# Kernel tuning notes

Measured on AMD Instinct MI355X. Metric: run time of the kernel, lower is better.

Reference implementation:

```python
import jax, jax.numpy as jnp
import numpy as np

B, S, D = 16, 2048, 400
HEADS, HEAD_SIZE = 4, 100
SCALE = 1.0 / np.float32(100.0 ** 0.5)


def setup_inputs() -> dict:
    key = jax.random.key(0)
    ks = jax.random.split(key, 8)
    return {
        "x": jax.random.normal(ks[0], (B, S, D), jnp.float32),
        "attn_kernel": jax.random.normal(ks[1], (3, D, HEAD_SIZE), jnp.float32) * 0.05,
        "attn_dense": jax.random.normal(ks[2], (D, HEADS * HEAD_SIZE), jnp.float32) * 0.05,
        "d1_w": jax.random.normal(ks[3], (400, 400), jnp.float32) * 0.05,
        "d1_b": jnp.zeros((400,), jnp.float32),
        "fc1_w": jax.random.normal(ks[4], (800, 512), jnp.float32) * 0.05,
        "fc1_b": jnp.zeros((512,), jnp.float32),
        "fc2_w": jax.random.normal(ks[5], (512, 256), jnp.float32) * 0.05,
        "fc2_b": jnp.zeros((256,), jnp.float32),
    }


def reference(x, attn_kernel, attn_dense, d1_w, d1_b, fc1_w, fc1_b, fc2_w, fc2_b):
    # Multi-head attention. NOTE: the original loops `heads` times over the SAME
    # shared kernel, so all 4 head outputs are identical; compute once, tile.
    WQ = jnp.einsum('bsd,dh->bsh', x, attn_kernel[0])  # [B,S,100]
    WK = jnp.einsum('bsd,dh->bsh', x, attn_kernel[1])
    WV = jnp.einsum('bsd,dh->bsh', x, attn_kernel[2])
    scores = jnp.einsum('bqh,bkh->bqk', WQ, WK) * SCALE  # [B,S,S]
    probs = jax.nn.softmax(scores, axis=-1)
    V = jnp.einsum('bqk,bkh->bqh', probs, WV)  # [B,S,100]
    out = jnp.tile(V, (1, 1, HEADS))  # concat of identical heads -> [B,S,400]
    out = jnp.einsum('bsd,de->bse', out, attn_dense)  # [B,S,400]
    # Dropout layers are identity at inference.
    h = jax.nn.relu(jnp.einsum('bsd,de->bse', out, d1_w) + d1_b)  # [B,S,400]
    pooled = jnp.concatenate([jnp.max(h, axis=1), jnp.mean(h, axis=1)], axis=-1)  # [B,800]
    h = jax.nn.relu(pooled @ fc1_w + fc1_b)  # [B,512]
    h = jax.nn.relu(h @ fc2_w + fc2_b)  # [B,256]
    return h
```

## Files before the change

### kernel.cpp

```cpp
#include <hip/hip_runtime.h>

typedef __attribute__((ext_vector_type(8))) _Float16 f16x8;
typedef __attribute__((ext_vector_type(4))) float f4v;
typedef __attribute__((ext_vector_type(8))) unsigned short us8;
typedef __attribute__((ext_vector_type(4))) unsigned short us4;
typedef unsigned short u16;

__device__ __forceinline__ u16 h2b(_Float16 h) { return __builtin_bit_cast(u16, h); }
__device__ __forceinline__ float b2f(u16 b) {
    return (float)__builtin_bit_cast(_Float16, b);
}

#define BAR() do { asm volatile("s_waitcnt lgkmcnt(0)" ::: "memory"); \
                   __builtin_amdgcn_s_barrier(); } while (0)

__global__ void k_w2p(const float* __restrict__ ad, const float* __restrict__ d1w,
                      float* __restrict__ w2p) {
    int i = blockIdx.x * 256 + threadIdx.x;
    if (i >= 51200) return;
    int es = blockIdx.y;
    int d = i / 400, j = i % 400;
    float acc = 0.f;
    if (d < 100) {
        const float* a0 = ad + d * 400 + es * 100;
        const float* wr = d1w + (es * 100) * 400 + j;
        #pragma unroll 4
        for (int e = 0; e < 100; ++e) {
            float av = a0[e] + a0[40000 + e] + a0[80000 + e] + a0[120000 + e];
            acc += av * wr[e * 400];
        }
    }
    w2p[es * 51200 + i] = acc;
}

__global__ void k_w2r(const float* __restrict__ w2p, u16* __restrict__ w2f) {
    int i = blockIdx.x * 256 + threadIdx.x;
    if (i >= 51200) return;
    float acc = w2p[i] + w2p[51200 + i] + w2p[102400 + i] + w2p[153600 + i];
    int d = i / 400, j = i % 400;
    int idx = ((j >> 4) * 4 + (d >> 5)) * 512 + (((d >> 3) & 3) * 16 + (j & 15)) * 8 + (d & 7);
    w2f[idx] = h2b((_Float16)acc);
}

__global__ void k_wprep(const float* __restrict__ ak, u16* __restrict__ wsp) {
    int i = blockIdx.x * 256 + threadIdx.x;
    if (i >= 159744) return;
    int k = i & 31, n = (i >> 5) & 127;
    int xx = i >> 12;
    int ks = xx % 13, m = xx / 13;
    int gk = ks * 32 + k;
    float v = (n < 100 && gk < 400) ? ak[m * 40000 + gk * 100 + n] : 0.f;
    _Float16 hb = (_Float16)v;
    _Float16 lb = (_Float16)(v - (float)hb);
    long base = (long)xx * 8192;
    int pos = n * 32 + ((((k >> 3) ^ (n & 3)) << 3) | (k & 7));
    wsp[base + pos] = h2b(hb);
    wsp[base + 4096 + pos] = h2b(lb);
}

__global__ __launch_bounds__(512) void k_gemm_qkv(
    const float* __restrict__ x, const u16* __restrict__ wsp,
    u16* __restrict__ QH, u16* __restrict__ KH, u16* __restrict__ VT) {
    __shared__ __align__(16) u16 smem[49152];

    const int tid = threadIdx.x;
    const int rowblk = blockIdx.x;
    const long row0 = (long)rowblk * 128;
    const int w = tid >> 6, l = tid & 63, g = l >> 4, c15 = l & 15;
    const int sr = tid >> 2, skc = tid & 3;

    f4v aQ[8], aK[8], aV[8];
    #pragma unroll
    for (int nt = 0; nt < 8; ++nt) {
        aQ[nt] = (f4v){0.f, 0.f, 0.f, 0.f};
        aK[nt] = (f4v){0.f, 0.f, 0.f, 0.f};
        aV[nt] = (f4v){0.f, 0.f, 0.f, 0.f};
    }

    const u16* wq  = wsp;
    const u16* wkh = wsp + 106496;
    const u16* wkl = wsp + 110592;
    const u16* wv  = wsp + 212992;

    float4 xr0, xr1;
    us8 wr[4];
    const int xpos = sr * 32 + ((skc * 8) ^ ((sr & 3) << 3));

    {
        const float* xp = x + (row0 + sr) * 400 + skc * 8;
        xr0 = *(const float4*)xp;
        xr1 = *(const float4*)(xp + 4);
        wr[0] = *(const us8*)&wq [(long)tid * 8];
        wr[1] = *(const us8*)&wkh[(long)tid * 8];
        wr[2] = *(const us8*)&wkl[(long)tid * 8];
        wr[3] = *(const us8*)&wv [(long)tid * 8];
        float va[8] = {xr0.x, xr0.y, xr0.z, xr0.w, xr1.x, xr1.y, xr1.z, xr1.w};
        us8 hi8, lo8;
        #pragma unroll
        for (int j = 0; j < 8; ++j) {
            _Float16 h = (_Float16)va[j];
            hi8[j] = h2b(h);
            lo8[j] = h2b((_Float16)(va[j] - (float)h));
        }
        *(us8*)&smem[xpos] = hi8;
        *(us8*)&smem[4096 + xpos] = lo8;
        *(us8*)&smem[8192  + tid * 8] = wr[0];
        *(us8*)&smem[12288 + tid * 8] = wr[1];
        *(us8*)&smem[16384 + tid * 8] = wr[2];
        *(us8*)&smem[20480 + tid * 8] = wr[3];
        const float* xp1 = x + (row0 + sr) * 400 + 32 + skc * 8;
        xr0 = *(const float4*)xp1;
        xr1 = *(const float4*)(xp1 + 4);
        wr[0] = *(const us8*)&wq [8192 + (long)tid * 8];
        wr[1] = *(const us8*)&wkh[8192 + (long)tid * 8];
        wr[2] = *(const us8*)&wkl[8192 + (long)tid * 8];
        wr[3] = *(const us8*)&wv [8192 + (long)tid * 8];
    }

    for (int ks = 0; ks < 13; ++ks) {
        BAR();
        u16* cb = smem + (ks & 1) * 24576;
        u16* sb = smem + ((ks & 1) ^ 1) * 24576;
        if (ks + 1 < 13) {
            float va[8] = {xr0.x, xr0.y, xr0.z, xr0.w, xr1.x, xr1.y, xr1.z, xr1.w};
            us8 hi8, lo8;
            #pragma unroll
            for (int j = 0; j < 8; ++j) {
                _Float16 h = (_Float16)va[j];
                hi8[j] = h2b(h);
                lo8[j] = h2b((_Float16)(va[j] - (float)h));
            }
            *(us8*)&sb[xpos] = hi8;
            *(us8*)&sb[4096 + xpos] = lo8;
            *(us8*)&sb[8192  + tid * 8] = wr[0];
            *(us8*)&sb[12288 + tid * 8] = wr[1];
            *(us8*)&sb[16384 + tid * 8] = wr[2];
            *(us8*)&sb[20480 + tid * 8] = wr[3];
            if (ks + 2 < 13) {
                if ((ks + 2) * 32 + skc * 8 < 400) {
                    const float* xp = x + (row0 + sr) * 400 + (ks + 2) * 32 + skc * 8;
                    xr0 = *(const float4*)xp;
                    xr1 = *(const float4*)(xp + 4);
                } else {
                    xr0 = make_float4(0.f, 0.f, 0.f, 0.f);
                    xr1 = make_float4(0.f, 0.f, 0.f, 0.f);
                }
                long wo = (long)(ks + 2) * 8192 + (long)tid * 8;
                wr[0] = *(const us8*)&wq [wo];
                wr[1] = *(const us8*)&wkh[wo];
                wr[2] = *(const us8*)&wkl[wo];
                wr[3] = *(const us8*)&wv [wo];
            }
        }
        const int arow = w * 16 + c15;
        const int axo = arow * 32 + ((g * 8) ^ ((arow & 3) << 3));
        f16x8 ah = *(const f16x8*)&cb[axo];
        f16x8 al = *(const f16x8*)&cb[4096 + axo];
        __builtin_amdgcn_s_setprio(1);
        #pragma unroll
        for (int nt = 0; nt < 8; ++nt) {
            int brow = nt * 16 + c15;
            int boff = brow * 32 + ((g * 8) ^ ((brow & 3) << 3));
            f16x8 qb = *(const f16x8*)&cb[8192 + boff];
            aQ[nt] = __builtin_amdgcn_mfma_f32_16x16x32_f16(ah, qb, aQ[nt], 0, 0, 0);
            aQ[nt] = __builtin_amdgcn_mfma_f32_16x16x32_f16(al, qb, aQ[nt], 0, 0, 0);
            f16x8 kh = *(const f16x8*)&cb[12288 + boff];
            aK[nt] = __builtin_amdgcn_mfma_f32_16x16x32_f16(ah, kh, aK[nt], 0, 0, 0);
            aK[nt] = __builtin_amdgcn_mfma_f32_16x16x32_f16(al, kh, aK[nt], 0, 0, 0);
            f16x8 kl = *(const f16x8*)&cb[16384 + boff];
            aK[nt] = __builtin_amdgcn_mfma_f32_16x16x32_f16(ah, kl, aK[nt], 0, 0, 0);
            f16x8 vb = *(const f16x8*)&cb[20480 + boff];
            aV[nt] = __builtin_amdgcn_mfma_f32_16x16x32_f16(ah, vb, aV[nt], 0, 0, 0);
            aV[nt] = __builtin_amdgcn_mfma_f32_16x16x32_f16(al, vb, aV[nt], 0, 0, 0);
        }
        __builtin_amdgcn_s_setprio(0);
    }
    BAR();
    u16* epi = smem;

    {
        const float qs = 0.14426950408889634f;
        #pragma unroll
        for (int nt = 0; nt < 8; ++nt) {
            #pragma unroll
            for (int r = 0; r < 4; ++r) {
                int row = w * 16 + 4 * g + r, col = nt * 16 + c15;
                epi[row * 128 + (col ^ ((row & 7) << 3))] =
                    h2b((_Float16)(aQ[nt][r] * qs));
            }
        }
        __syncthreads();
        #pragma unroll
        for (int r = 0; r < 4; ++r) {
            int u = tid + r * 512;
            int row = u >> 4, c = u & 15;
            *(us8*)&QH[(row0 + row) * 128 + c * 8] =
                *(const us8*)&epi[row * 128 + ((c * 8) ^ ((row & 7) << 3))];
        }
        __syncthreads();
    }
    {
        #pragma unroll
        for (int nt = 0; nt < 8; ++nt) {
            #pragma unroll
            for (int r = 0; r < 4; ++r) {
                int row = w * 16 + 4 * g + r, col = nt * 16 + c15;
                epi[row * 128 + (col ^ ((row & 7) << 3))] = h2b((_Float16)aK[nt][r]);
            }
        }
        __syncthreads();
        u16* dst = KH + (long)rowblk * 16384;
        #pragma unroll
        for (int r = 0; r < 4; ++r) {
            int u = tid + r * 512;
            *(us8*)&dst[(long)u * 8] = *(const us8*)&epi[u * 8];
        }
        __syncthreads();
    }
    {
        const int q0 = w * 16 + 4 * g;
        const int vtile = q0 >> 6, q0w = q0 & 63;
        #pragma unroll
        for (int nt = 0; nt < 8; ++nt) {
            int d = nt * 16 + c15;
            if (d < 112) {
                us4 v4;
                #pragma unroll
                for (int r = 0; r < 4; ++r) v4[r] = h2b((_Float16)aV[nt][r]);
                *(us4*)&epi[vtile * 8192 + d * 64 + (q0w ^ ((d & 7) << 3))] = v4;
            }
        }
        __syncthreads();
        #pragma unroll
        for (int r = 0; r < 4; ++r) {
            int u = tid + r * 512;
            int vt2 = u >> 10, uu = u & 1023;
            if (uu < 896)
                *(us8*)&VT[((long)(2 * rowblk + vt2)) * 7168 + (long)uu * 8] =
                    *(const us8*)&epi[u * 8];
        }
    }
}

__global__ __launch_bounds__(512) void k_flash(
    const u16* __restrict__ Qg, const u16* __restrict__ Kg,
    const u16* __restrict__ Vg, u16* __restrict__ VOI,
    float* __restrict__ ML) {
    __shared__ __align__(16) char smem[69632];

    const int tid = threadIdx.x;
    const int w = tid >> 6, l = tid & 63, g = (l >> 4) & 3, c15 = l & 15;
    const int qg = w & 3, kh = w >> 2;
    const int b = blockIdx.y, qt = blockIdx.x, half = blockIdx.z;
    const int t0 = half * 16;

    const u16* qp = Qg + ((long)b * 2048 + qt * 64 + qg * 16 + c15) * 128;
    f16x8 qh[4];
    #pragma unroll
    for (int ks = 0; ks < 4; ++ks) qh[ks] = *(const f16x8*)(qp + ks * 32 + g * 8);

    f4v O[7];
    #pragma unroll
    for (int i = 0; i < 7; ++i) O[i] = (f4v){0.f, 0.f, 0.f, 0.f};
    float lrow = 0.f;

    const char* Kb = (const char*)(Kg + (long)b * 32 * 8192);
    const char* Vb = (const char*)(Vg + (long)b * 32 * 7168);
    char* Pw = smem + 61440 + w * 1024;

    us8 kreg[2], vreg[2];
    #pragma unroll
    for (int r = 0; r < 2; ++r) {
        int u = tid + r * 512;
        kreg[r] = *(const us8*)(Kb + (long)t0 * 16384 + (long)u * 16);
        if (u < 896) vreg[r] = *(const us8*)(Vb + (long)t0 * 14336 + (long)u * 16);
    }
    #pragma unroll
    for (int r = 0; r < 2; ++r) {
        int u = tid + r * 512;
        *(us8*)(smem + u * 16) = kreg[r];
        if (u < 896) *(us8*)(smem + 32768 + u * 16) = vreg[r];
    }
    #pragma unroll
    for (int r = 0; r < 2; ++r) {
        int u = tid + r * 512;
        kreg[r] = *(const us8*)(Kb + (long)(t0 + 1) * 16384 + (long)u * 16);
        if (u < 896) vreg[r] = *(const us8*)(Vb + (long)(t0 + 1) * 14336 + (long)u * 16);
    }

    for (int t = t0; t < t0 + 16; ++t) {
        const int cur = (t - t0) & 1;
        BAR();
        if (t + 1 < t0 + 16) {
            #pragma unroll
            for (int r = 0; r < 2; ++r) {
                int u = tid + r * 512;
                *(us8*)(smem + (cur ^ 1) * 16384 + u * 16) = kreg[r];
                if (u < 896)
                    *(us8*)(smem + 32768 + (cur ^ 1) * 14336 + u * 16) = vreg[r];
            }
            if (t + 2 < t0 + 16) {
                #pragma unroll
                for (int r = 0; r < 2; ++r) {
                    int u = tid + r * 512;
                    kreg[r] = *(const us8*)(Kb + (long)(t + 2) * 16384 + (long)u * 16);
                    if (u < 896)
                        vreg[r] = *(const us8*)(Vb + (long)(t + 2) * 14336 + (long)u * 16);
                }
            }
        }
        const char* Kc = smem + cur * 16384;
        const char* Vc = smem + 32768 + cur * 14336;

        f4v s[2];
        s[0] = (f4v){0.f, 0.f, 0.f, 0.f};
        s[1] = (f4v){0.f, 0.f, 0.f, 0.f};
        __builtin_amdgcn_s_setprio(1);
        #pragma unroll
        for (int ks = 0; ks < 4; ++ks) {
            #pragma unroll
            for (int nt = 0; nt < 2; ++nt) {
                int key = kh * 32 + nt * 16 + c15;
                f16x8 kf = *(const f16x8*)(Kc + key * 256 +
                                           ((ks * 64 + g * 16) ^ ((key & 7) << 4)));
                s[nt] = __builtin_amdgcn_mfma_f32_16x16x32_f16(kf, qh[ks], s[nt], 0, 0, 0);
            }
        }
        __builtin_amdgcn_s_setprio(0);

        {
            float sum = 0.f;
            #pragma unroll
            for (int nt = 0; nt < 2; ++nt) {
                #pragma unroll
                for (int r = 0; r < 4; ++r) {
                    float p = exp2f(s[nt][r]);
                    s[nt][r] = p;
                    sum += p;
                }
            }
            sum += __shfl_xor(sum, 16);
            sum += __shfl_xor(sum, 32);
            lrow += sum;
        }

        #pragma unroll
        for (int nt = 0; nt < 2; ++nt) {
            uint2 pw2;
            pw2.x = __builtin_bit_cast(unsigned int,
                        __builtin_amdgcn_cvt_pkrtz(s[nt][0], s[nt][1]));
            pw2.y = __builtin_bit_cast(unsigned int,
                        __builtin_amdgcn_cvt_pkrtz(s[nt][2], s[nt][3]));
            *(uint2*)(Pw + c15 * 64 + ((nt * 32 + g * 8) ^ ((c15 & 3) << 4))) = pw2;
        }
        __builtin_amdgcn_s_setprio(1);
        f16x8 pa = *(const f16x8*)(Pw + c15 * 64 + ((g * 16) ^ ((c15 & 3) << 4)));
        #pragma unroll
        for (int dt = 0; dt < 7; ++dt) {
            int d = dt * 16 + c15;
            f16x8 vf = *(const f16x8*)(Vc + d * 128 +
                                       ((kh * 64 + g * 16) ^ ((d & 7) << 4)));
            O[dt] = __builtin_amdgcn_mfma_f32_16x16x32_f16(pa, vf, O[dt], 0, 0, 0);
        }
        __builtin_amdgcn_s_setprio(0);
    }

    float* PSf = (float*)Pw;
    if (g == 0) PSf[c15] = lrow;
    BAR();
    if (kh == 1) {
        char* ex = smem + qg * 7168;
        #pragma unroll
        for (int dt = 0; dt < 7; ++dt)
            *(f4v*)(ex + (dt * 64 + l) * 16) = O[dt];
    }
    BAR();
    if (kh == 0) {
        const char* ex = smem + qg * 7168;
        #pragma unroll
        for (int dt = 0; dt < 7; ++dt)
            O[dt] += *(const f4v*)(ex + (dt * 64 + l) * 16);
        const float* PSp = (const float*)(smem + 61440 + (w + 4) * 1024);
        float linv[4];
        #pragma unroll
        for (int r = 0; r < 4; ++r)
            linv[r] = 1.f / (PSf[4 * g + r] + PSp[4 * g + r]);
        if (g == 0) {
            long mbase = (long)half * 32768 + b * 2048 + qt * 64 + qg * 16;
            ML[mbase + c15] = PSf[c15] + PSp[c15];
        }
        u16* vout = VOI + ((long)(half * 16 + b) * 2048 + qt * 64 + qg * 16) * 112;
        #pragma unroll
        for (int r = 0; r < 4; ++r) {
            int row = 4 * g + r;
            #pragma unroll
            for (int dt = 0; dt < 7; ++dt)
                vout[row * 112 + dt * 16 + c15] =
                    h2b((_Float16)(O[dt][r] * linv[r]));
        }
    }
}

__global__ __launch_bounds__(256) void k_hpool(
    const u16* __restrict__ VOI, const float* __restrict__ ML,
    const u16* __restrict__ W2F, const float* __restrict__ d1b,
    float* __restrict__ pmax, float* __restrict__ psum) {
    __shared__ __align__(16) u16 A[8192];
    __shared__ float redM[4][400], redS[4][400];
    __shared__ float wgt[64][2];
    const int tid = threadIdx.x;
    const int w = tid >> 6, l = tid & 63, g = l >> 4, c15 = l & 15;
    const int b = blockIdx.y, rt = blockIdx.x;

    if (tid < 64) {
        float a = ML[b * 2048 + rt * 64 + tid];
        float c = ML[32768 + b * 2048 + rt * 64 + tid];
        float inv = 1.f / (a + c);
        wgt[tid][0] = a * inv;
        wgt[tid][1] = c * inv;
    }
    if (tid < 128) {
        int r = tid >> 1, c = 14 + (tid & 1);
        us8 z = {0, 0, 0, 0, 0, 0, 0, 0};
        *(us8*)&A[r * 128 + ((c * 8) ^ ((r & 7) << 3))] = z;
    }
    __syncthreads();

    const u16* s1 = VOI + ((long)b * 2048 + rt * 64) * 112;
    const u16* s2 = VOI + ((long)(16 + b) * 2048 + rt * 64) * 112;
    #pragma unroll
    for (int r = 0; r < 4; ++r) {
        int u = tid + r * 256;
        if (u < 896) {
            int row = u / 14, c = u % 14;
            us8 p1 = *(const us8*)&s1[row * 112 + c * 8];
            us8 p2 = *(const us8*)&s2[row * 112 + c * 8];
            float w1 = wgt[row][0], w2 = wgt[row][1];
            us8 o;
            #pragma unroll
            for (int j = 0; j < 8; ++j)
                o[j] = h2b((_Float16)(w1 * b2f(p1[j]) + w2 * b2f(p2[j])));
            *(us8*)&A[row * 128 + ((c * 8) ^ ((row & 7) << 3))] = o;
        }
    }
    __syncthreads();

    const int arow = w * 16 + c15;
    f16x8 af[4];
    #pragma unroll
    for (int ks = 0; ks < 4; ++ks)
        af[ks] = *(const f16x8*)&A[arow * 128 + ((ks * 32 + g * 8) ^ ((arow & 7) << 3))];

    for (int nt = 0; nt < 25; ++nt) {
        f4v acc = (f4v){0.f, 0.f, 0.f, 0.f};
        #pragma unroll
        for (int ks = 0; ks < 4; ++ks) {
            f16x8 bf = *(const f16x8*)&W2F[(nt * 4 + ks) * 512 + l * 8];
            acc = __builtin_amdgcn_mfma_f32_16x16x32_f16(af[ks], bf, acc, 0, 0, 0);
        }
        float bias = d1b[nt * 16 + c15];
        float mx4 = -1e30f, sm4 = 0.f;
        #pragma unroll
        for (int r = 0; r < 4; ++r) {
            float h = fmaxf(acc[r] + bias, 0.f);
            mx4 = fmaxf(mx4, h);
            sm4 += h;
        }
        mx4 = fmaxf(mx4, __shfl_xor(mx4, 16));
        mx4 = fmaxf(mx4, __shfl_xor(mx4, 32));
        sm4 += __shfl_xor(sm4, 16);
        sm4 += __shfl_xor(sm4, 32);
        if (g == 0) {
            redM[w][nt * 16 + c15] = mx4;
            redS[w][nt * 16 + c15] = sm4;
        }
    }
    __syncthreads();
    for (int j = tid; j < 400; j += 256) {
        float mx = fmaxf(fmaxf(redM[0][j], redM[1][j]), fmaxf(redM[2][j], redM[3][j]));
        float sm = redS[0][j] + redS[1][j] + redS[2][j] + redS[3][j];
        pmax[((long)b * 32 + rt) * 400 + j] = mx;
        psum[((long)b * 32 + rt) * 400 + j] = sm;
    }
}

__global__ __launch_bounds__(256) void k_pred(
    const float* __restrict__ pmax, const float* __restrict__ psum,
    float* __restrict__ pooled) {
    __shared__ float rm[16][17], rs[16][17];
    const int b = blockIdx.x, jt = blockIdx.y, tid = threadIdx.x;
    const int jo = tid & 15, ts = tid >> 4;
    const int j = jt * 16 + jo;
    float mx = -1e30f, sm = 0.f;
    for (int t = ts; t < 32; t += 16) {
        mx = fmaxf(mx, pmax[((long)b * 32 + t) * 400 + j]);
        sm += psum[((long)b * 32 + t) * 400 + j];
    }
    rm[ts][jo] = mx; rs[ts][jo] = sm;
    __syncthreads();
    if (tid < 16) {
        float m2 = rm[0][tid], s2 = rs[0][tid];
        #pragma unroll
        for (int t = 1; t < 16; ++t) { m2 = fmaxf(m2, rm[t][tid]); s2 += rs[t][tid]; }
        pooled[b * 800 + jt * 16 + tid] = m2;
        pooled[b * 800 + 400 + jt * 16 + tid] = s2 * (1.f / 2048.f);
    }
}

__global__ __launch_bounds__(256) void k_fc1(
    const float* __restrict__ pooled, const float* __restrict__ w,
    const float* __restrict__ bias, float* __restrict__ out) {
    __shared__ float pl[800];
    __shared__ float red[16][17];
    const int b = blockIdx.x, jt = blockIdx.y, tid = threadIdx.x;
    const int jo = tid & 15, ks = tid >> 4;
    const int j = jt * 16 + jo;
    for (int i = tid; i < 800; i += 256) pl[i] = pooled[b * 800 + i];
    __syncthreads();
    float acc = 0.f;
    #pragma unroll 5
    for (int kk = 0; kk < 50; ++kk) {
        int k = ks * 50 + kk;
        acc += pl[k] * w[k * 512 + j];
    }
    red[ks][jo] = acc;
    __syncthreads();
    if (tid < 16) {
        float s = red[0][tid];
        #pragma unroll
        for (int t = 1; t < 16; ++t) s += red[t][tid];
        out[b * 512 + jt * 16 + tid] = fmaxf(s + bias[jt * 16 + tid], 0.f);
    }
}

__global__ __launch_bounds__(256) void k_fc2(
    const float* __restrict__ h, const float* __restrict__ w,
    const float* __restrict__ bias, float* __restrict__ out) {
    __shared__ float hl[512];
    __shared__ float red[16][17];
    const int b = blockIdx.x, jt = blockIdx.y, tid = threadIdx.x;
    const int jo = tid & 15, ks = tid >> 4;
    const int j = jt * 16 + jo;
    for (int i = tid; i < 512; i += 256) hl[i] = h[b * 512 + i];
    __syncthreads();
    float acc = 0.f;
    #pragma unroll 4
    for (int kk = 0; kk < 32; ++kk) {
        int k = ks * 32 + kk;
        acc += hl[k] * w[k * 256 + j];
    }
    red[ks][jo] = acc;
    __syncthreads();
    if (tid < 16) {
        float s = red[0][tid];
        #pragma unroll
        for (int t = 1; t < 16; ++t) s += red[t][tid];
        out[b * 256 + jt * 16 + tid] = fmaxf(s + bias[jt * 16 + tid], 0.f);
    }
}

extern "C" void kernel_launch(void* const* d_in, const int* in_sizes, int n_in,
                              void* d_out, int out_size, void* d_ws, size_t ws_size,
                              hipStream_t stream) {
    const float* x          = (const float*)d_in[0];
    const float* attn_kernel= (const float*)d_in[1];
    const float* attn_dense = (const float*)d_in[2];
    const float* d1_w       = (const float*)d_in[3];
    const float* d1_b       = (const float*)d_in[4];
    const float* fc1_w      = (const float*)d_in[5];
    const float* fc1_b      = (const float*)d_in[6];
    const float* fc2_w      = (const float*)d_in[7];
    const float* fc2_b      = (const float*)d_in[8];
    float* out = (float*)d_out;
    char*  wsb = (char*)d_ws;

    u16*    QH   = (u16*)(wsb);
    u16*    KH   = (u16*)(wsb + 8388608);
    u16*    VT   = (u16*)(wsb + 16777216);
    u16*    VOI  = (u16*)(wsb + 24117248);
    u16*    WSP  = (u16*)(wsb + 38797312);
    u16*    W2F  = (u16*)(wsb + 39436288);
    float*  PMAX = (float*)(wsb + 39538688);
    float*  PSUM = (float*)(wsb + 40357888);
    float*  ML   = (float*)(wsb + 41177088);
    float*  W2P  = (float*)(wsb + 41439232);
    float*  POOL = (float*)(wsb + 42258432);
    float*  FC1  = (float*)(wsb + 42309632);

    k_wprep<<<624, 256, 0, stream>>>(attn_kernel, WSP);
    k_w2p <<<dim3(200, 4), 256, 0, stream>>>(attn_dense, d1_w, W2P);
    k_w2r <<<200, 256, 0, stream>>>(W2P, W2F);
    k_gemm_qkv<<<256, 512, 0, stream>>>(x, WSP, QH, KH, VT);
    k_flash<<<dim3(32, 16, 2), 512, 0, stream>>>(QH, KH, VT, VOI, ML);
    k_hpool<<<dim3(32, 16), 256, 0, stream>>>(VOI, ML, W2F, d1_b, PMAX, PSUM);
    k_pred<<<dim3(16, 25), 256, 0, stream>>>(PMAX, PSUM, POOL);
    k_fc1 <<<dim3(16, 32), 256, 0, stream>>>(POOL, fc1_w, fc1_b, FC1);
    k_fc2 <<<dim3(16, 16), 256, 0, stream>>>(FC1, fc2_w, fc2_b, out);
}
```

Measured before the change: 145.8 us.

## Give each flash wave its own 16 query rows over full key tiles

The flash kernel now assigns each of the 8 waves a distinct 16-row query group covering all 64 keys of each tile, so a block handles 128 queries instead of 64. The grid is halved. This doubles reuse of every K/V tile staged in LDS and removes the cross-wave split-key reduction, its extra barriers and the LDS exchange at the end. In exchange each wave carries more score registers and does twice the MFMA work per tile. Fewer blocks (512) may reduce occupancy across the CUs.

```diff
diff --git a/kernel.cpp b/kernel.cpp
--- a/kernel.cpp
+++ b/kernel.cpp
@@ -246,15 +246,16 @@
     const u16* __restrict__ Qg, const u16* __restrict__ Kg,
     const u16* __restrict__ Vg, u16* __restrict__ VOI,
     float* __restrict__ ML) {
-    __shared__ __align__(16) char smem[69632];
+    __shared__ __align__(16) char KS[2][16384];
+    __shared__ __align__(16) char VS[2][14336];
+    __shared__ __align__(16) char PS[8][2048];
 
     const int tid = threadIdx.x;
-    const int w = tid >> 6, l = tid & 63, g = (l >> 4) & 3, c15 = l & 15;
-    const int qg = w & 3, kh = w >> 2;
+    const int w = tid >> 6, l = tid & 63, g = l >> 4, c15 = l & 15;
     const int b = blockIdx.y, qt = blockIdx.x, half = blockIdx.z;
     const int t0 = half * 16;
 
-    const u16* qp = Qg + ((long)b * 2048 + qt * 64 + qg * 16 + c15) * 128;
+    const u16* qp = Qg + ((long)b * 2048 + qt * 128 + w * 16 + c15) * 128;
     f16x8 qh[4];
     #pragma unroll
     for (int ks = 0; ks < 4; ++ks) qh[ks] = *(const f16x8*)(qp + ks * 32 + g * 8);
@@ -266,7 +267,7 @@
 
     const char* Kb = (const char*)(Kg + (long)b * 32 * 8192);
     const char* Vb = (const char*)(Vg + (long)b * 32 * 7168);
-    char* Pw = smem + 61440 + w * 1024;
+    char* Pw = PS[w];
 
     us8 kreg[2], vreg[2];
     #pragma unroll
@@ -278,8 +279,8 @@
     #pragma unroll
     for (int r = 0; r < 2; ++r) {
         int u = tid + r * 512;
-        *(us8*)(smem + u * 16) = kreg[r];
-        if (u < 896) *(us8*)(smem + 32768 + u * 16) = vreg[r];
+        *(us8*)(KS[0] + u * 16) = kreg[r];
+        if (u < 896) *(us8*)(VS[0] + u * 16) = vreg[r];
     }
     #pragma unroll
     for (int r = 0; r < 2; ++r) {
@@ -295,9 +296,8 @@
             #pragma unroll
             for (int r = 0; r < 2; ++r) {
                 int u = tid + r * 512;
-                *(us8*)(smem + (cur ^ 1) * 16384 + u * 16) = kreg[r];
-                if (u < 896)
-                    *(us8*)(smem + 32768 + (cur ^ 1) * 14336 + u * 16) = vreg[r];
+                *(us8*)(KS[cur ^ 1] + u * 16) = kreg[r];
+                if (u < 896) *(us8*)(VS[cur ^ 1] + u * 16) = vreg[r];
             }
             if (t + 2 < t0 + 16) {
                 #pragma unroll
@@ -309,18 +309,18 @@
                 }
             }
         }
-        const char* Kc = smem + cur * 16384;
-        const char* Vc = smem + 32768 + cur * 14336;
-
-        f4v s[2];
-        s[0] = (f4v){0.f, 0.f, 0.f, 0.f};
-        s[1] = (f4v){0.f, 0.f, 0.f, 0.f};
+        const char* Kc = KS[cur];
+        const char* Vc = VS[cur];
+
+        f4v s[4];
+        #pragma unroll
+        for (int nt = 0; nt < 4; ++nt) s[nt] = (f4v){0.f, 0.f, 0.f, 0.f};
         __builtin_amdgcn_s_setprio(1);
         #pragma unroll
         for (int ks = 0; ks < 4; ++ks) {
             #pragma unroll
-            for (int nt = 0; nt < 2; ++nt) {
-                int key = kh * 32 + nt * 16 + c15;
+            for (int nt = 0; nt < 4; ++nt) {
+                int key = nt * 16 + c15;
                 f16x8 kf = *(const f16x8*)(Kc + key * 256 +
                                            ((ks * 64 + g * 16) ^ ((key & 7) << 4)));
                 s[nt] = __builtin_amdgcn_mfma_f32_16x16x32_f16(kf, qh[ks], s[nt], 0, 0, 0);
@@ -328,76 +328,60 @@
         }
         __builtin_amdgcn_s_setprio(0);
 
-        {
-            float sum = 0.f;
-            #pragma unroll
-            for (int nt = 0; nt < 2; ++nt) {
-                #pragma unroll
-                for (int r = 0; r < 4; ++r) {
-                    float p = exp2f(s[nt][r]);
-                    s[nt][r] = p;
-                    sum += p;
-                }
-            }
-            sum += __shfl_xor(sum, 16);
-            sum += __shfl_xor(sum, 32);
-            lrow += sum;
-        }
-
-        #pragma unroll
-        for (int nt = 0; nt < 2; ++nt) {
+        float sum = 0.f;
+        #pragma unroll
+        for (int nt = 0; nt < 4; ++nt) {
+            #pragma unroll
+            for (int r = 0; r < 4; ++r) {
+                float p = exp2f(s[nt][r]);
+                s[nt][r] = p;
+                sum += p;
+            }
+        }
+        sum += __shfl_xor(sum, 16);
+        sum += __shfl_xor(sum, 32);
+        lrow += sum;
+
+        #pragma unroll
+        for (int nt = 0; nt < 4; ++nt) {
             uint2 pw2;
             pw2.x = __builtin_bit_cast(unsigned int,
                         __builtin_amdgcn_cvt_pkrtz(s[nt][0], s[nt][1]));
             pw2.y = __builtin_bit_cast(unsigned int,
                         __builtin_amdgcn_cvt_pkrtz(s[nt][2], s[nt][3]));
-            *(uint2*)(Pw + c15 * 64 + ((nt * 32 + g * 8) ^ ((c15 & 3) << 4))) = pw2;
+            *(uint2*)(Pw + c15 * 128 + ((32 * nt + 8 * g) ^ ((c15 & 7) << 4))) = pw2;
         }
         __builtin_amdgcn_s_setprio(1);
-        f16x8 pa = *(const f16x8*)(Pw + c15 * 64 + ((g * 16) ^ ((c15 & 3) << 4)));
-        #pragma unroll
-        for (int dt = 0; dt < 7; ++dt) {
-            int d = dt * 16 + c15;
-            f16x8 vf = *(const f16x8*)(Vc + d * 128 +
-                                       ((kh * 64 + g * 16) ^ ((d & 7) << 4)));
-            O[dt] = __builtin_amdgcn_mfma_f32_16x16x32_f16(pa, vf, O[dt], 0, 0, 0);
+        #pragma unroll
+        for (int k0 = 0; k0 < 2; ++k0) {
+            f16x8 pa = *(const f16x8*)(Pw + c15 * 128 +
+                                       ((k0 * 64 + g * 16) ^ ((c15 & 7) << 4)));
+            #pragma unroll
+            for (int dt = 0; dt < 7; ++dt) {
+                int d = dt * 16 + c15;
+                f16x8 vf = *(const f16x8*)(Vc + d * 128 +
+                                           ((k0 * 64 + g * 16) ^ ((d & 7) << 4)));
+                O[dt] = __builtin_amdgcn_mfma_f32_16x16x32_f16(pa, vf, O[dt], 0, 0, 0);
+            }
         }
         __builtin_amdgcn_s_setprio(0);
     }
 
-    float* PSf = (float*)Pw;
-    if (g == 0) PSf[c15] = lrow;
-    BAR();
-    if (kh == 1) {
-        char* ex = smem + qg * 7168;
+    if (g == 0) {
+        ((float*)Pw)[c15] = lrow;
+        ML[half * 32768 + b * 2048 + qt * 128 + w * 16 + c15] = lrow;
+    }
+    float linv[4];
+    #pragma unroll
+    for (int r = 0; r < 4; ++r) linv[r] = 1.f / ((float*)Pw)[4 * g + r];
+    u16* vout = VOI + ((long)(half * 16 + b) * 2048 + qt * 128 + w * 16) * 112;
+    #pragma unroll
+    for (int r = 0; r < 4; ++r) {
+        int row = 4 * g + r;
         #pragma unroll
         for (int dt = 0; dt < 7; ++dt)
-            *(f4v*)(ex + (dt * 64 + l) * 16) = O[dt];
-    }
-    BAR();
-    if (kh == 0) {
-        const char* ex = smem + qg * 7168;
-        #pragma unroll
-        for (int dt = 0; dt < 7; ++dt)
-            O[dt] += *(const f4v*)(ex + (dt * 64 + l) * 16);
-        const float* PSp = (const float*)(smem + 61440 + (w + 4) * 1024);
-        float linv[4];
-        #pragma unroll
-        for (int r = 0; r < 4; ++r)
-            linv[r] = 1.f / (PSf[4 * g + r] + PSp[4 * g + r]);
-        if (g == 0) {
-            long mbase = (long)half * 32768 + b * 2048 + qt * 64 + qg * 16;
-            ML[mbase + c15] = PSf[c15] + PSp[c15];
-        }
-        u16* vout = VOI + ((long)(half * 16 + b) * 2048 + qt * 64 + qg * 16) * 112;
-        #pragma unroll
-        for (int r = 0; r < 4; ++r) {
-            int row = 4 * g + r;
-            #pragma unroll
-            for (int dt = 0; dt < 7; ++dt)
-                vout[row * 112 + dt * 16 + c15] =
-                    h2b((_Float16)(O[dt][r] * linv[r]));
-        }
+            vout[row * 112 + dt * 16 + c15] =
+                h2b((_Float16)(O[dt][r] * linv[r]));
     }
 }
 
@@ -591,7 +575,7 @@
     k_w2p <<<dim3(200, 4), 256, 0, stream>>>(attn_dense, d1_w, W2P);
     k_w2r <<<200, 256, 0, stream>>>(W2P, W2F);
     k_gemm_qkv<<<256, 512, 0, stream>>>(x, WSP, QH, KH, VT);
-    k_flash<<<dim3(32, 16, 2), 512, 0, stream>>>(QH, KH, VT, VOI, ML);
+    k_flash<<<dim3(16, 16, 2), 512, 0, stream>>>(QH, KH, VT, VOI, ML);
     k_hpool<<<dim3(32, 16), 256, 0, stream>>>(VOI, ML, W2F, d1_b, PMAX, PSUM);
     k_pred<<<dim3(16, 25), 256, 0, stream>>>(PMAX, PSUM, POOL);
     k_fc1 <<<dim3(16, 32), 256, 0, stream>>>(POOL, fc1_w, fc1_b, FC1);
```

After: 137.2 us. -5.9%, faster.
